# Kernel optimization log

Hardware: AMD Instinct MI355X
Metric: run time of the kernel (lower is better)

The kernel has to match this reference:

```python
import jax, jax.numpy as jnp
import numpy as np

D_MODEL, H, DH = 1024, 16, 64
S, B, LCACHE = 16, 8, 8192
W_SCALE = 0.02  # keep pre-softmax logits in a sane range


def setup_inputs() -> dict:
    key = jax.random.key(0)
    ks = jax.random.split(key, 7)
    return {
        "x": jax.random.normal(ks[0], (S, B, D_MODEL), jnp.float32),
        "cache_k": jax.random.normal(ks[1], (LCACHE, B, H, DH), jnp.float32),
        "cache_v": jax.random.normal(ks[2], (LCACHE, B, H, DH), jnp.float32),
        "Wq": jax.random.normal(ks[3], (D_MODEL, H * DH), jnp.float32) * W_SCALE,
        "Wk": jax.random.normal(ks[4], (D_MODEL, H * DH), jnp.float32) * W_SCALE,
        "Wv": jax.random.normal(ks[5], (D_MODEL, H * DH), jnp.float32) * W_SCALE,
        "Wo": jax.random.normal(ks[6], (H * DH, D_MODEL), jnp.float32) * W_SCALE,
    }


def reference(x, cache_k, cache_v, Wq, Wk, Wv, Wo):
    S, B, D = x.shape
    Lc, _, H, Dh = cache_k.shape
    # project and split heads: (S, B, H, Dh)
    q = (x @ Wq).reshape(S, B, H, Dh)
    k_new = (x @ Wk).reshape(S, B, H, Dh)
    v_new = (x @ Wv).reshape(S, B, H, Dh)
    # extend cache along time axis -> (L, B, H, Dh), L = Lc + S
    new_k = jnp.concatenate([cache_k, k_new], axis=0)
    new_v = jnp.concatenate([cache_v, v_new], axis=0)
    L = Lc + S
    scale = 1.0 / jnp.sqrt(jnp.asarray(Dh, x.dtype))
    # scores: (B, H, S, L)
    scores = jnp.einsum('sbhd,tbhd->bhst', q, new_k) * scale
    # causal: query at position Lc+s attends to key positions t <= Lc+s
    mask = jnp.arange(L)[None, :] <= (Lc + jnp.arange(S))[:, None]  # (S, L)
    scores = jnp.where(mask[None, None], scores, jnp.asarray(-1e9, scores.dtype))
    attn = jax.nn.softmax(scores, axis=-1)
    ctx = jnp.einsum('bhst,tbhd->sbhd', attn, new_v).reshape(S, B, H * Dh)
    res = ctx @ Wo  # (S, B, D)
    return res, new_k, new_v
```

## Files before the change

### kernel.cpp

```cpp
#include <hip/hip_runtime.h>
#include <hip/hip_bf16.h>

#define S 16
#define B 8
#define H 16
#define DH 64
#define D 1024
#define HD 1024
#define LC 8192
#define LMAX (LC + S)
#define NCH 32
#define CHT 256
#define TILE 16
#define NT (CHT / TILE)

typedef __attribute__((ext_vector_type(4))) float f4;
typedef __attribute__((ext_vector_type(4))) short s4v;
typedef __attribute__((ext_vector_type(8))) short s8v;

__device__ inline short bfs(float f) {
    __hip_bfloat16 h = __float2bfloat16(f);
    return __builtin_bit_cast(short, h);
}
__device__ inline s4v pack4(float a, float b, float c, float d) {
    s4v r; r[0] = bfs(a); r[1] = bfs(b); r[2] = bfs(c); r[3] = bfs(d); return r;
}

__global__ __launch_bounds__(256) void proj_qkv(const float* __restrict__ x,
        const float* __restrict__ Wq, const float* __restrict__ Wk,
        const float* __restrict__ Wv,
        float* __restrict__ q_ws, float* __restrict__ newk, float* __restrict__ newv,
        float* __restrict__ res)
{
    int bx = blockIdx.x;
    int rg  = bx / 12;
    int rem = bx % 12;
    int mat = rem >> 2, chunk = rem & 3;
    int o = chunk * 256 + threadIdx.x;
    const float* W  = (mat == 0) ? Wq : ((mat == 1) ? Wk : Wv);
    const float* xr = x + (size_t)rg * 4 * D;

    float a0 = 0.f, a1 = 0.f, a2 = 0.f, a3 = 0.f;
    #pragma unroll 16
    for (int d = 0; d < D; ++d) {
        float w = W[(size_t)d * HD + o];
        a0 += xr[d] * w;
        a1 += xr[D + d] * w;
        a2 += xr[2 * D + d] * w;
        a3 += xr[3 * D + d] * w;
    }
    float acc[4] = {a0, a1, a2, a3};
    #pragma unroll
    for (int i = 0; i < 4; ++i) {
        int row = rg * 4 + i;
        int s = row >> 3, b = row & 7;
        if (mat == 0) {
            q_ws[(size_t)row * HD + o] = acc[i];
            res[(size_t)row * D + o] = 0.f;
        } else {
            float* dst = (mat == 1) ? newk : newv;
            dst[(size_t)((LC + s) * B + b) * HD + o] = acc[i];
        }
    }
}

__global__ __launch_bounds__(256, 4) void attn_fused(const float* __restrict__ q_ws,
        const float* __restrict__ cache_k, const float* __restrict__ cache_v,
        float* __restrict__ newk, float* __restrict__ newv,
        float* __restrict__ m_part, float* __restrict__ l_part,
        float* __restrict__ pv_part)
{
    extern __shared__ char smem[];
    short* Ksp = (short*)smem;
    short* Vp  = Ksp + TILE * 256;

    int bx = blockIdx.x;
    int chunk = bx & 31;
    int hgb = bx >> 5;
    int hg = hgb & 3, b = hgb >> 2;
    int tid = threadIdx.x, l = tid & 63, wid = tid >> 6;
    int g = l >> 4, c16 = l & 15;
    int h = hg * 4 + wid;
    int rrb = tid >> 6, ch = tid & 63;
    int w = ch >> 4, cc = ch & 15;
    unsigned vbase = (unsigned)(uintptr_t)Vp + (unsigned)wid * 2112u;

    s8v qf[2];
    {
        const float* qp = q_ws + ((size_t)(c16 * B + b)) * HD + h * DH + g * 8;
        #pragma unroll
        for (int sl = 0; sl < 2; ++sl) {
            float4 qa = *(const float4*)(qp + sl * 32);
            float4 qb = *(const float4*)(qp + sl * 32 + 4);
            s8v q;
            q[0] = bfs(qa.x * 0.125f); q[1] = bfs(qa.y * 0.125f);
            q[2] = bfs(qa.z * 0.125f); q[3] = bfs(qa.w * 0.125f);
            q[4] = bfs(qb.x * 0.125f); q[5] = bfs(qb.y * 0.125f);
            q[6] = bfs(qb.z * 0.125f); q[7] = bfs(qb.w * 0.125f);
            qf[sl] = q;
        }
    }

    float m_prev = -1e30f, l_acc = 0.f;
    f4 acc[4] = {{0,0,0,0},{0,0,0,0},{0,0,0,0},{0,0,0,0}};

    int t0base = chunk * CHT;
    int sw = (c16 & 7) << 3;
    size_t cbase = (size_t)b * 1024 + hg * 256 + ch * 4;

    f4 kb[2][4], vb[2][4];
    #pragma unroll
    for (int gg = 0; gg < 4; ++gg) {
        size_t off = ((size_t)(t0base + rrb + 4 * gg)) * 8192 + cbase;
        kb[0][gg] = __builtin_nontemporal_load((const f4*)(cache_k + off));
        vb[0][gg] = __builtin_nontemporal_load((const f4*)(cache_v + off));
    }

    #pragma unroll
    for (int it = 0; it < NT; ++it) {
        const int cur = it & 1, nxt = cur ^ 1;
        int t0 = t0base + it * TILE;

        if (it + 1 < NT) {
            #pragma unroll
            for (int gg = 0; gg < 4; ++gg) {
                size_t off = ((size_t)(t0 + TILE + rrb + 4 * gg)) * 8192 + cbase;
                kb[nxt][gg] = __builtin_nontemporal_load((const f4*)(cache_k + off));
                vb[nxt][gg] = __builtin_nontemporal_load((const f4*)(cache_v + off));
            }
        }
        asm volatile("s_waitcnt lgkmcnt(0)" ::: "memory");
        __builtin_amdgcn_s_barrier();
        __builtin_amdgcn_sched_barrier(0);

        #pragma unroll
        for (int gg = 0; gg < 4; ++gg) {
            int rr = rrb + 4 * gg;
            size_t off = ((size_t)(t0 + rr)) * 8192 + cbase;
            __builtin_nontemporal_store(kb[cur][gg], (f4*)(newk + off));
            __builtin_nontemporal_store(vb[cur][gg], (f4*)(newv + off));
            int kidx = rr * 256 + w * 64 + ((cc * 4) ^ ((rr & 7) << 3));
            *(s4v*)(Ksp + kidx) = pack4(kb[cur][gg][0], kb[cur][gg][1], kb[cur][gg][2], kb[cur][gg][3]);
            int vidx = w * 1056 + (cc >> 2) * 264 + (rr >> 2) * 64 + (rr & 3) * 16 + (cc & 3) * 4;
            *(s4v*)(Vp + vidx) = pack4(vb[cur][gg][0], vb[cur][gg][1], vb[cur][gg][2], vb[cur][gg][3]);
        }
        asm volatile("s_waitcnt lgkmcnt(0)" ::: "memory");
        __builtin_amdgcn_s_barrier();
        __builtin_amdgcn_sched_barrier(0);

        f4 d0 = {0,0,0,0};
        #pragma unroll
        for (int sl = 0; sl < 2; ++sl) {
            int col = (sl * 32 + g * 8) ^ sw;
            s8v k0 = *(const s8v*)(Ksp + c16 * 256 + wid * 64 + col);
            d0 = __builtin_amdgcn_mfma_f32_16x16x32_bf16(k0, qf[sl], d0, 0, 0, 0);
        }
        float hm = fmaxf(fmaxf(d0[0], d0[1]), fmaxf(d0[2], d0[3]));
        hm = fmaxf(hm, __shfl_xor(hm, 16));
        hm = fmaxf(hm, __shfl_xor(hm, 32));
        float mn = fmaxf(m_prev, hm);
        float sf = __expf(m_prev - mn);
        m_prev = mn;
        f4 p0;
        #pragma unroll
        for (int r = 0; r < 4; ++r) p0[r] = __expf(d0[r] - mn);
        float rs = (p0[0] + p0[1]) + (p0[2] + p0[3]);
        rs += __shfl_xor(rs, 16);
        rs += __shfl_xor(rs, 32);
        l_acc = l_acc * sf + rs;
        #pragma unroll
        for (int dd = 0; dd < 4; ++dd) acc[dd] *= sf;

        s4v pb0 = pack4(p0[0], p0[1], p0[2], p0[3]);
        s4v vfr[4];
        #pragma unroll
        for (int dd = 0; dd < 4; ++dd) {
            unsigned adr = vbase + 2u * (unsigned)(dd * 264 + g * 64 + c16);
            asm volatile("ds_read_b64_tr_b16 %0, %1" : "=v"(vfr[dd]) : "v"(adr));
        }
        asm volatile("s_waitcnt lgkmcnt(0)" ::: "memory");
        __builtin_amdgcn_sched_barrier(0);
        #pragma unroll
        for (int dd = 0; dd < 4; ++dd)
            acc[dd] = __builtin_amdgcn_mfma_f32_16x16x16bf16_1k(vfr[dd], pb0, acc[dd], 0, 0, 0);
    }

    if (chunk == NCH - 1) {
        __syncthreads();
        #pragma unroll
        for (int q = 0; q < 4; ++q) {
            int idx = tid + q * 256;
            int rr = idx >> 6, c2 = idx & 63;
            int w2 = c2 >> 4, cc2 = c2 & 15;
            size_t off = ((size_t)(LC + rr)) * 8192 + (size_t)b * 1024 + hg * 256 + c2 * 4;
            float4 k4 = *(const float4*)(newk + off);
            float4 v4 = *(const float4*)(newv + off);
            int kidx = rr * 256 + w2 * 64 + ((cc2 * 4) ^ ((rr & 7) << 3));
            *(s4v*)(Ksp + kidx) = pack4(k4.x, k4.y, k4.z, k4.w);
            int vidx = w2 * 1056 + (cc2 >> 2) * 264 + (rr >> 2) * 64 + (rr & 3) * 16 + (cc2 & 3) * 4;
            *(s4v*)(Vp + vidx) = pack4(v4.x, v4.y, v4.z, v4.w);
        }
        __syncthreads();
        f4 d0 = {0,0,0,0};
        #pragma unroll
        for (int sl = 0; sl < 2; ++sl) {
            int col = (sl * 32 + g * 8) ^ sw;
            s8v k0 = *(const s8v*)(Ksp + c16 * 256 + wid * 64 + col);
            d0 = __builtin_amdgcn_mfma_f32_16x16x32_bf16(k0, qf[sl], d0, 0, 0, 0);
        }
        #pragma unroll
        for (int r = 0; r < 4; ++r)
            if (4 * g + r > c16) d0[r] = -1e30f;
        float hm = fmaxf(fmaxf(d0[0], d0[1]), fmaxf(d0[2], d0[3]));
        hm = fmaxf(hm, __shfl_xor(hm, 16));
        hm = fmaxf(hm, __shfl_xor(hm, 32));
        float mn = fmaxf(m_prev, hm);
        float sf = __expf(m_prev - mn);
        m_prev = mn;
        f4 p0;
        #pragma unroll
        for (int r = 0; r < 4; ++r) p0[r] = __expf(d0[r] - mn);
        float rs = (p0[0] + p0[1]) + (p0[2] + p0[3]);
        rs += __shfl_xor(rs, 16);
        rs += __shfl_xor(rs, 32);
        l_acc = l_acc * sf + rs;
        #pragma unroll
        for (int dd = 0; dd < 4; ++dd) acc[dd] *= sf;
        s4v pb0 = pack4(p0[0], p0[1], p0[2], p0[3]);
        s4v vfr[4];
        #pragma unroll
        for (int dd = 0; dd < 4; ++dd) {
            unsigned adr = vbase + 2u * (unsigned)(dd * 264 + g * 64 + c16);
            asm volatile("ds_read_b64_tr_b16 %0, %1" : "=v"(vfr[dd]) : "v"(adr));
        }
        asm volatile("s_waitcnt lgkmcnt(0)" ::: "memory");
        __builtin_amdgcn_sched_barrier(0);
        #pragma unroll
        for (int dd = 0; dd < 4; ++dd)
            acc[dd] = __builtin_amdgcn_mfma_f32_16x16x16bf16_1k(vfr[dd], pb0, acc[dd], 0, 0, 0);
    }

    int pi = ((b * 16 + h) * NCH) + chunk;
    #pragma unroll
    for (int dd = 0; dd < 4; ++dd)
        #pragma unroll
        for (int r = 0; r < 4; ++r)
            pv_part[((size_t)pi * 64 + dd * 16 + g * 4 + r) * 16 + c16] = acc[dd][r];
    if (l < 16) {
        m_part[pi * 16 + l] = m_prev;
        l_part[pi * 16 + l] = l_acc;
    }
}

__global__ __launch_bounds__(256) void combine_proj(const float* __restrict__ m_part,
        const float* __restrict__ l_part, const float* __restrict__ pv_part,
        const float* __restrict__ Wo, float* __restrict__ res)
{
    __shared__ float wexp[NCH][16];
    __shared__ float Ls[16];
    __shared__ float cds[64][16];
    int bx = blockIdx.x;
    int oc = bx & 3, bh = bx >> 2;
    int h = bh & 15, b = bh >> 4;
    int tid = threadIdx.x;

    if (tid < 16) {
        int s = tid;
        float M = -1e30f;
        #pragma unroll
        for (int c = 0; c < NCH; ++c) M = fmaxf(M, m_part[(bh * NCH + c) * 16 + s]);
        float L = 0.f;
        #pragma unroll
        for (int c = 0; c < NCH; ++c) {
            float e = __expf(m_part[(bh * NCH + c) * 16 + s] - M);
            wexp[c][s] = e;
            L += e * l_part[(bh * NCH + c) * 16 + s];
        }
        Ls[s] = L;
    }
    __syncthreads();
    #pragma unroll
    for (int k = 0; k < 4; ++k) {
        int idx = tid + k * 256;
        int d = idx >> 4, s = idx & 15;
        float v = 0.f;
        #pragma unroll
        for (int c = 0; c < NCH; ++c)
            v += wexp[c][s] * pv_part[((size_t)(bh * NCH + c) * 64 + d) * 16 + s];
        cds[d][s] = v / Ls[s];
    }
    __syncthreads();

    int o = oc * 256 + tid;
    float acc[16];
    #pragma unroll
    for (int s = 0; s < 16; ++s) acc[s] = 0.f;
    #pragma unroll 8
    for (int d = 0; d < 64; ++d) {
        float wv = Wo[(size_t)(h * 64 + d) * D + o];
        #pragma unroll
        for (int q = 0; q < 4; ++q) {
            f4 cq = *(const f4*)&cds[d][q * 4];
            acc[q * 4 + 0] += cq[0] * wv;
            acc[q * 4 + 1] += cq[1] * wv;
            acc[q * 4 + 2] += cq[2] * wv;
            acc[q * 4 + 3] += cq[3] * wv;
        }
    }
    #pragma unroll
    for (int s = 0; s < 16; ++s)
        atomicAdd(res + (size_t)(s * B + b) * D + o, acc[s]);
}

extern "C" void kernel_launch(void* const* d_in, const int* in_sizes, int n_in,
                              void* d_out, int out_size, void* d_ws, size_t ws_size,
                              hipStream_t stream)
{
    const float* x  = (const float*)d_in[0];
    const float* ck = (const float*)d_in[1];
    const float* cv = (const float*)d_in[2];
    const float* Wq = (const float*)d_in[3];
    const float* Wk = (const float*)d_in[4];
    const float* Wv = (const float*)d_in[5];
    const float* Wo = (const float*)d_in[6];

    float* out  = (float*)d_out;
    float* res  = out;
    float* newk = out + (size_t)S * B * D;
    float* newv = newk + (size_t)LMAX * B * H * DH;

    float* q_ws    = (float*)d_ws;
    float* ctx     = q_ws + (size_t)S * B * HD;
    float* m_part  = ctx + (size_t)S * B * HD;
    float* l_part  = m_part + (size_t)B * H * NCH * S;
    float* pv_part = l_part + (size_t)B * H * NCH * S;

    size_t smem = (size_t)(TILE * 256 + 4 * 1056) * 2;

    hipLaunchKernelGGL(proj_qkv, dim3(32 * 12), dim3(256), 0, stream,
                       x, Wq, Wk, Wv, q_ws, newk, newv, res);
    hipLaunchKernelGGL(attn_fused, dim3(B * 4 * NCH), dim3(256), smem, stream,
                       q_ws, ck, cv, newk, newv, m_part, l_part, pv_part);
    hipLaunchKernelGGL(combine_proj, dim3(B * H * 4), dim3(256), 0, stream,
                       m_part, l_part, pv_part, Wo, res);
}
```

Baseline: 295.4 us.

## Double-buffer LDS tiles in attention and widen QKV projection rows per block

The attention kernel now keeps two LDS buffers, so the next tile is staged into one while the current tile is computed from the other. This removes one barrier per iteration and lets global loads run two tiles ahead. Compute is wrapped in raised wave priority, and launch bounds drop from 4 to 3 blocks per CU to make room for the larger LDS footprint. Separately, the QKV projection computes 8 rows per thread instead of 4 using half as many blocks, which halves weight reads but also reduces parallelism.

After: 380.1 us. 28.7% more time.

```diff
diff --git a/kernel.cpp b/kernel.cpp
--- a/kernel.cpp
+++ b/kernel.cpp
@@ -13,6 +13,7 @@
 #define CHT 256
 #define TILE 16
 #define NT (CHT / TILE)
+#define BUFS 8320
 
 typedef __attribute__((ext_vector_type(4))) float f4;
 typedef __attribute__((ext_vector_type(4))) short s4v;
@@ -38,21 +39,20 @@
     int mat = rem >> 2, chunk = rem & 3;
     int o = chunk * 256 + threadIdx.x;
     const float* W  = (mat == 0) ? Wq : ((mat == 1) ? Wk : Wv);
-    const float* xr = x + (size_t)rg * 4 * D;
-
-    float a0 = 0.f, a1 = 0.f, a2 = 0.f, a3 = 0.f;
+    const float* xr = x + (size_t)rg * 8 * D;
+
+    float acc[8];
+    #pragma unroll
+    for (int i = 0; i < 8; ++i) acc[i] = 0.f;
     #pragma unroll 16
     for (int d = 0; d < D; ++d) {
         float w = W[(size_t)d * HD + o];
-        a0 += xr[d] * w;
-        a1 += xr[D + d] * w;
-        a2 += xr[2 * D + d] * w;
-        a3 += xr[3 * D + d] * w;
-    }
-    float acc[4] = {a0, a1, a2, a3};
-    #pragma unroll
-    for (int i = 0; i < 4; ++i) {
-        int row = rg * 4 + i;
+        #pragma unroll
+        for (int i = 0; i < 8; ++i) acc[i] += xr[(size_t)i * D + d] * w;
+    }
+    #pragma unroll
+    for (int i = 0; i < 8; ++i) {
+        int row = rg * 8 + i;
         int s = row >> 3, b = row & 7;
         if (mat == 0) {
             q_ws[(size_t)row * HD + o] = acc[i];
@@ -64,15 +64,17 @@
     }
 }
 
-__global__ __launch_bounds__(256, 4) void attn_fused(const float* __restrict__ q_ws,
+__global__ __launch_bounds__(256, 3) void attn_fused(const float* __restrict__ q_ws,
         const float* __restrict__ cache_k, const float* __restrict__ cache_v,
         float* __restrict__ newk, float* __restrict__ newv,
         float* __restrict__ m_part, float* __restrict__ l_part,
         float* __restrict__ pv_part)
 {
-    extern __shared__ char smem[];
-    short* Ksp = (short*)smem;
-    short* Vp  = Ksp + TILE * 256;
+    extern __shared__ short smem_s[];
+    short* K0 = smem_s;
+    short* V0 = smem_s + 4096;
+    short* K1 = smem_s + BUFS;
+    short* V1 = smem_s + BUFS + 4096;
 
     int bx = blockIdx.x;
     int chunk = bx & 31;
@@ -83,7 +85,6 @@
     int h = hg * 4 + wid;
     int rrb = tid >> 6, ch = tid & 63;
     int w = ch >> 4, cc = ch & 15;
-    unsigned vbase = (unsigned)(uintptr_t)Vp + (unsigned)wid * 2112u;
 
     s8v qf[2];
     {
@@ -109,51 +110,41 @@
     size_t cbase = (size_t)b * 1024 + hg * 256 + ch * 4;
 
     f4 kb[2][4], vb[2][4];
-    #pragma unroll
-    for (int gg = 0; gg < 4; ++gg) {
-        size_t off = ((size_t)(t0base + rrb + 4 * gg)) * 8192 + cbase;
-        kb[0][gg] = __builtin_nontemporal_load((const f4*)(cache_k + off));
-        vb[0][gg] = __builtin_nontemporal_load((const f4*)(cache_v + off));
-    }
-
-    #pragma unroll
-    for (int it = 0; it < NT; ++it) {
-        const int cur = it & 1, nxt = cur ^ 1;
-        int t0 = t0base + it * TILE;
-
-        if (it + 1 < NT) {
-            #pragma unroll
-            for (int gg = 0; gg < 4; ++gg) {
-                size_t off = ((size_t)(t0 + TILE + rrb + 4 * gg)) * 8192 + cbase;
-                kb[nxt][gg] = __builtin_nontemporal_load((const f4*)(cache_k + off));
-                vb[nxt][gg] = __builtin_nontemporal_load((const f4*)(cache_v + off));
-            }
-        }
-        asm volatile("s_waitcnt lgkmcnt(0)" ::: "memory");
-        __builtin_amdgcn_s_barrier();
-        __builtin_amdgcn_sched_barrier(0);
-
+
+    auto load_tile = [&](int t0, f4 (&kg)[4], f4 (&vg)[4]) {
+        #pragma unroll
+        for (int gg = 0; gg < 4; ++gg) {
+            size_t off = ((size_t)(t0 + rrb + 4 * gg)) * 8192 + cbase;
+            kg[gg] = __builtin_nontemporal_load((const f4*)(cache_k + off));
+            vg[gg] = __builtin_nontemporal_load((const f4*)(cache_v + off));
+        }
+    };
+    auto stage_tile = [&](short* Kb, short* Vb, int t0, f4 (&kg)[4], f4 (&vg)[4]) {
         #pragma unroll
         for (int gg = 0; gg < 4; ++gg) {
             int rr = rrb + 4 * gg;
             size_t off = ((size_t)(t0 + rr)) * 8192 + cbase;
-            __builtin_nontemporal_store(kb[cur][gg], (f4*)(newk + off));
-            __builtin_nontemporal_store(vb[cur][gg], (f4*)(newv + off));
+            __builtin_nontemporal_store(kg[gg], (f4*)(newk + off));
+            __builtin_nontemporal_store(vg[gg], (f4*)(newv + off));
             int kidx = rr * 256 + w * 64 + ((cc * 4) ^ ((rr & 7) << 3));
-            *(s4v*)(Ksp + kidx) = pack4(kb[cur][gg][0], kb[cur][gg][1], kb[cur][gg][2], kb[cur][gg][3]);
+            *(s4v*)(Kb + kidx) = pack4(kg[gg][0], kg[gg][1], kg[gg][2], kg[gg][3]);
             int vidx = w * 1056 + (cc >> 2) * 264 + (rr >> 2) * 64 + (rr & 3) * 16 + (cc & 3) * 4;
-            *(s4v*)(Vp + vidx) = pack4(vb[cur][gg][0], vb[cur][gg][1], vb[cur][gg][2], vb[cur][gg][3]);
-        }
-        asm volatile("s_waitcnt lgkmcnt(0)" ::: "memory");
-        __builtin_amdgcn_s_barrier();
-        __builtin_amdgcn_sched_barrier(0);
-
+            *(s4v*)(Vb + vidx) = pack4(vg[gg][0], vg[gg][1], vg[gg][2], vg[gg][3]);
+        }
+    };
+    auto compute_tile = [&](short* Kb, short* Vb, bool causal) {
+        __builtin_amdgcn_s_setprio(1);
         f4 d0 = {0,0,0,0};
         #pragma unroll
         for (int sl = 0; sl < 2; ++sl) {
             int col = (sl * 32 + g * 8) ^ sw;
-            s8v k0 = *(const s8v*)(Ksp + c16 * 256 + wid * 64 + col);
+            s8v k0 = *(const s8v*)(Kb + c16 * 256 + wid * 64 + col);
             d0 = __builtin_amdgcn_mfma_f32_16x16x32_bf16(k0, qf[sl], d0, 0, 0, 0);
+        }
+        if (causal) {
+            #pragma unroll
+            for (int r = 0; r < 4; ++r)
+                if (4 * g + r > c16) d0[r] = -1e30f;
         }
         float hm = fmaxf(fmaxf(d0[0], d0[1]), fmaxf(d0[2], d0[3]));
         hm = fmaxf(hm, __shfl_xor(hm, 16));
@@ -172,10 +163,11 @@
         for (int dd = 0; dd < 4; ++dd) acc[dd] *= sf;
 
         s4v pb0 = pack4(p0[0], p0[1], p0[2], p0[3]);
+        unsigned vb_ = (unsigned)(uintptr_t)Vb + (unsigned)wid * 2112u;
         s4v vfr[4];
         #pragma unroll
         for (int dd = 0; dd < 4; ++dd) {
-            unsigned adr = vbase + 2u * (unsigned)(dd * 264 + g * 64 + c16);
+            unsigned adr = vb_ + 2u * (unsigned)(dd * 264 + g * 64 + c16);
             asm volatile("ds_read_b64_tr_b16 %0, %1" : "=v"(vfr[dd]) : "v"(adr));
         }
         asm volatile("s_waitcnt lgkmcnt(0)" ::: "memory");
@@ -183,6 +175,34 @@
         #pragma unroll
         for (int dd = 0; dd < 4; ++dd)
             acc[dd] = __builtin_amdgcn_mfma_f32_16x16x16bf16_1k(vfr[dd], pb0, acc[dd], 0, 0, 0);
+        __builtin_amdgcn_s_setprio(0);
+    };
+
+    load_tile(t0base, kb[0], vb[0]);
+    stage_tile(K0, V0, t0base, kb[0], vb[0]);
+    load_tile(t0base + TILE, kb[1], vb[1]);
+    asm volatile("s_waitcnt lgkmcnt(0)" ::: "memory");
+    __builtin_amdgcn_s_barrier();
+    __builtin_amdgcn_sched_barrier(0);
+
+    #pragma unroll
+    for (int it = 0; it < NT; ++it) {
+        const int cur = it & 1, nxt = cur ^ 1;
+        short* Kc = cur ? K1 : K0;
+        short* Vc = cur ? V1 : V0;
+        short* Kn = cur ? K0 : K1;
+        short* Vn = cur ? V0 : V1;
+
+        compute_tile(Kc, Vc, false);
+
+        if (it + 1 < NT) {
+            stage_tile(Kn, Vn, t0base + (it + 1) * TILE, kb[nxt], vb[nxt]);
+            if (it + 2 < NT)
+                load_tile(t0base + (it + 2) * TILE, kb[cur], vb[cur]);
+        }
+        asm volatile("s_waitcnt lgkmcnt(0)" ::: "memory");
+        __builtin_amdgcn_s_barrier();
+        __builtin_amdgcn_sched_barrier(0);
     }
 
     if (chunk == NCH - 1) {
@@ -196,48 +216,12 @@
             float4 k4 = *(const float4*)(newk + off);
             float4 v4 = *(const float4*)(newv + off);
             int kidx = rr * 256 + w2 * 64 + ((cc2 * 4) ^ ((rr & 7) << 3));
-            *(s4v*)(Ksp + kidx) = pack4(k4.x, k4.y, k4.z, k4.w);
+            *(s4v*)(K0 + kidx) = pack4(k4.x, k4.y, k4.z, k4.w);
             int vidx = w2 * 1056 + (cc2 >> 2) * 264 + (rr >> 2) * 64 + (rr & 3) * 16 + (cc2 & 3) * 4;
-            *(s4v*)(Vp + vidx) = pack4(v4.x, v4.y, v4.z, v4.w);
+            *(s4v*)(V0 + vidx) = pack4(v4.x, v4.y, v4.z, v4.w);
         }
         __syncthreads();
-        f4 d0 = {0,0,0,0};
-        #pragma unroll
-        for (int sl = 0; sl < 2; ++sl) {
-            int col = (sl * 32 + g * 8) ^ sw;
-            s8v k0 = *(const s8v*)(Ksp + c16 * 256 + wid * 64 + col);
-            d0 = __builtin_amdgcn_mfma_f32_16x16x32_bf16(k0, qf[sl], d0, 0, 0, 0);
-        }
-        #pragma unroll
-        for (int r = 0; r < 4; ++r)
-            if (4 * g + r > c16) d0[r] = -1e30f;
-        float hm = fmaxf(fmaxf(d0[0], d0[1]), fmaxf(d0[2], d0[3]));
-        hm = fmaxf(hm, __shfl_xor(hm, 16));
-        hm = fmaxf(hm, __shfl_xor(hm, 32));
-        float mn = fmaxf(m_prev, hm);
-        float sf = __expf(m_prev - mn);
-        m_prev = mn;
-        f4 p0;
-        #pragma unroll
-        for (int r = 0; r < 4; ++r) p0[r] = __expf(d0[r] - mn);
-        float rs = (p0[0] + p0[1]) + (p0[2] + p0[3]);
-        rs += __shfl_xor(rs, 16);
-        rs += __shfl_xor(rs, 32);
-        l_acc = l_acc * sf + rs;
-        #pragma unroll
-        for (int dd = 0; dd < 4; ++dd) acc[dd] *= sf;
-        s4v pb0 = pack4(p0[0], p0[1], p0[2], p0[3]);
-        s4v vfr[4];
-        #pragma unroll
-        for (int dd = 0; dd < 4; ++dd) {
-            unsigned adr = vbase + 2u * (unsigned)(dd * 264 + g * 64 + c16);
-            asm volatile("ds_read_b64_tr_b16 %0, %1" : "=v"(vfr[dd]) : "v"(adr));
-        }
-        asm volatile("s_waitcnt lgkmcnt(0)" ::: "memory");
-        __builtin_amdgcn_sched_barrier(0);
-        #pragma unroll
-        for (int dd = 0; dd < 4; ++dd)
-            acc[dd] = __builtin_amdgcn_mfma_f32_16x16x16bf16_1k(vfr[dd], pb0, acc[dd], 0, 0, 0);
+        compute_tile(K0, V0, true);
     }
 
     int pi = ((b * 16 + h) * NCH) + chunk;
@@ -335,9 +319,9 @@
     float* l_part  = m_part + (size_t)B * H * NCH * S;
     float* pv_part = l_part + (size_t)B * H * NCH * S;
 
-    size_t smem = (size_t)(TILE * 256 + 4 * 1056) * 2;
-
-    hipLaunchKernelGGL(proj_qkv, dim3(32 * 12), dim3(256), 0, stream,
+    size_t smem = (size_t)BUFS * 2 * 2;
+
+    hipLaunchKernelGGL(proj_qkv, dim3(16 * 12), dim3(256), 0, stream,
                        x, Wq, Wk, Wv, q_ws, newk, newv, res);
     hipLaunchKernelGGL(attn_fused, dim3(B * 4 * NCH), dim3(256), smem, stream,
                        q_ws, ck, cv, newk, newv, m_part, l_part, pv_part);
```
